# Kernel optimization log

Hardware: AMD Instinct MI355X
Metric: run time of the kernel (lower is better)

The kernel has to match this reference:

```python
import jax, jax.numpy as jnp
import numpy as np

C, INTER, RED4 = 256, 128, 64  # in_channels, inter_ch=max(C//2,32), C//4

def setup_inputs() -> dict:
    key = jax.random.key(0)
    ks = jax.random.split(key, 12)
    B, H, W = 8, 64, 64
    s = 0.02
    return {
        "x": jax.random.normal(ks[0], (B, C, H, W), dtype=jnp.float32),
        "theta_w": jax.random.normal(ks[1], (INTER, C), dtype=jnp.float32) * s,
        "phi_w": jax.random.normal(ks[2], (INTER, C), dtype=jnp.float32) * s,
        "g_w": jax.random.normal(ks[3], (INTER, C), dtype=jnp.float32) * s,
        "out_w": jax.random.normal(ks[4], (C, INTER), dtype=jnp.float32) * s,
        "bn_gamma": jnp.ones((C,), dtype=jnp.float32),
        "bn_beta": jnp.zeros((C,), dtype=jnp.float32),
        "fc1_w": jax.random.normal(ks[5], (RED4, C), dtype=jnp.float32) * s,
        "fc1_b": jnp.zeros((RED4,), dtype=jnp.float32),
        "fc2_w": jax.random.normal(ks[6], (C, RED4), dtype=jnp.float32) * s,
        "fc2_b": jnp.zeros((C,), dtype=jnp.float32),
    }

def reference(x, theta_w, phi_w, g_w, out_w, bn_gamma, bn_beta, fc1_w, fc1_b, fc2_w, fc2_b):
    B, Cc, H, W = x.shape
    N = H * W
    xf = x.reshape(B, Cc, N)                              # [B,C,N]
    # 1x1 convs == per-pixel matmuls
    theta = jnp.einsum('ic,bcn->bni', theta_w, xf)        # [B,N,I]
    phi = jnp.einsum('ic,bcn->bin', phi_w, xf)            # [B,I,N]
    g = jnp.einsum('ic,bcn->bni', g_w, xf)                # [B,N,I]
    scale = 1.0 / jnp.sqrt(jnp.asarray(theta.shape[-1], theta.dtype))
    attn = jax.nn.softmax(jnp.einsum('bni,bim->bnm', theta, phi) * scale, axis=-1)  # [B,N,N]
    out = jnp.einsum('bnm,bmi->bni', attn, g)             # [B,N,I]
    out = jnp.einsum('ci,bni->bcn', out_w, out).reshape(B, Cc, H, W)
    # BatchNorm2d (training mode: batch stats, biased variance, eps=1e-5)
    mean = out.mean(axis=(0, 2, 3))
    var = out.var(axis=(0, 2, 3))
    out = (out - mean[:, None, None]) * jax.lax.rsqrt(var[:, None, None] + 1e-5)
    out = out * bn_gamma[:, None, None] + bn_beta[:, None, None]
    # SE channel attention on the input x
    pooled = x.mean(axis=(2, 3))                          # [B,C]
    h = jax.nn.relu(pooled @ fc1_w.T + fc1_b)
    ch_w = jax.nn.sigmoid(h @ fc2_w.T + fc2_b)[:, :, None, None]
    return x + out * ch_w
```

## Files before the change

kernel.cpp:

```cpp
#include <hip/hip_runtime.h>

#define B_DIM 8
#define C_DIM 256
#define I_DIM 128
#define N_DIM 4096
#define R_DIM 64

typedef unsigned short u16;
typedef unsigned int u32;
typedef __attribute__((ext_vector_type(8))) __bf16 bf16x8;
typedef __attribute__((ext_vector_type(4))) float f32x4;
typedef __attribute__((ext_vector_type(16))) float f32x16;

union BF8 { u32 u[4]; bf16x8 v; };

__device__ __forceinline__ u16 f2bf(float f) {
    union { float f; u32 u; } v; v.f = f;
    u32 r = v.u + 0x7FFFu + ((v.u >> 16) & 1u);
    return (u16)(r >> 16);
}
__device__ __forceinline__ float bf2f(u16 h) {
    union { u32 u; float f; } v; v.u = (u32)h << 16; return v.f;
}
__device__ __forceinline__ u32 pk2(float a, float b) {
    return (u32)f2bf(a) | ((u32)f2bf(b) << 16);
}
__device__ __forceinline__ void async16(const u16* g, u16* l) {
    __builtin_amdgcn_global_load_lds((const __attribute__((address_space(1))) void*)g,
                                     (__attribute__((address_space(3))) void*)l, 16, 0, 0);
}

#define TH_SCALE 0.1275204890136f

static constexpr size_t OFF_BNSUM = 0;
static constexpr size_t OFF_BNSQ  = 1024;
static constexpr size_t OFF_POOL  = 2048;
static constexpr size_t OFF_CHW   = 10240;
static constexpr size_t OFF_W3    = 18432;
static constexpr size_t OFF_OWB   = 215040;
static constexpr size_t OFF_AO0   = 280576;
static constexpr size_t OFF_AO1   = OFF_AO0 + 8388608;
static constexpr size_t OFF_THETA = OFF_AO1 + 8388608;
static constexpr size_t OFF_PHIT  = OFF_THETA + 8388608;
static constexpr size_t OFF_GT    = OFF_PHIT + 8388608;
static constexpr size_t OFF_L0    = OFF_GT + 8388608;
static constexpr size_t OFF_L1    = OFF_L0 + 131072;
static constexpr size_t OFF_OUT2  = OFF_L1 + 131072;

__global__ void prep_kernel(const float* __restrict__ tw, const float* __restrict__ pw,
                            const float* __restrict__ gw, const float* __restrict__ ow,
                            u16* __restrict__ w3, u16* __restrict__ owb,
                            float* __restrict__ bnzero) {
    int idx = blockIdx.x * 256 + threadIdx.x;
    if (idx < 512) bnzero[idx] = 0.f;
    if (idx < 3 * 32768) {
        const float* src = idx < 32768 ? tw : (idx < 65536 ? pw : gw);
        w3[idx] = f2bf(src[idx & 32767]);
    }
    if (idx < 32768) owb[idx] = f2bf(ow[idx]);
}

__global__ void pool_kernel(const float* __restrict__ x, float* __restrict__ pooled) {
    int bc = blockIdx.x;
    const float4* row = (const float4*)(x + (size_t)bc * N_DIM);
    int t = threadIdx.x;
    float s = 0.f;
    for (int it = 0; it < 4; ++it) {
        float4 v = row[t + it * 256];
        s += v.x + v.y + v.z + v.w;
    }
    for (int d = 32; d; d >>= 1) s += __shfl_down(s, d);
    __shared__ float ls[4];
    if ((t & 63) == 0) ls[t >> 6] = s;
    __syncthreads();
    if (t == 0) pooled[bc] = (ls[0] + ls[1] + ls[2] + ls[3]) * (1.f / N_DIM);
}

__global__ void se_kernel(const float* __restrict__ pooled,
                          const float* __restrict__ fc1w, const float* __restrict__ fc1b,
                          const float* __restrict__ fc2w, const float* __restrict__ fc2b,
                          float* __restrict__ chw) {
    int b = blockIdx.x, t = threadIdx.x;
    __shared__ float sp[C_DIM], sh[R_DIM];
    sp[t] = pooled[b * C_DIM + t];
    __syncthreads();
    if (t < R_DIM) {
        float a = fc1b[t];
        for (int c = 0; c < C_DIM; ++c) a += sp[c] * fc1w[t * C_DIM + c];
        sh[t] = a > 0.f ? a : 0.f;
    }
    __syncthreads();
    float a = fc2b[t];
    for (int j = 0; j < R_DIM; ++j) a += sh[j] * fc2w[t * R_DIM + j];
    chw[b * C_DIM + t] = 1.f / (1.f + __builtin_amdgcn_exp2f(-a * 1.44269504089f));
}

__global__ __launch_bounds__(256) void qkv_kernel(const float* __restrict__ x,
                                                  const u16* __restrict__ w3,
                                                  u16* __restrict__ theta,
                                                  u16* __restrict__ phiT,
                                                  u16* __restrict__ gT) {
    const int bid = blockIdx.x;
    const int b = bid & 7, nt = bid >> 3;
    const int n0 = nt * 64;
    const int t = threadIdx.x, lane = t & 63, w = t >> 6;
    const int cl = lane & 31, h = lane >> 5;

    __shared__ u16 As[64 * 256];
    __shared__ u16 Ep[128 * 72];

    {
        const float* xb = x + ((size_t)b * C_DIM) * N_DIM + n0;
        for (int it = 0; it < 16; ++it) {
            int id = it * 256 + t;
            int c = id >> 4, l16 = id & 15;
            float4 v = *(const float4*)(xb + (size_t)c * N_DIM + l16 * 4);
            int g = c >> 3, co = c & 7;
            float vv[4] = {v.x, v.y, v.z, v.w};
            #pragma unroll
            for (int k = 0; k < 4; ++k) {
                int n = l16 * 4 + k;
                As[n * 256 + ((g ^ (n & 7)) << 3) + co] = f2bf(vv[k]);
            }
        }
    }
    __syncthreads();

    const int mt = w & 1;
    const int ip = w >> 1;
    bf16x8 afr[16];
    #pragma unroll
    for (int ks = 0; ks < 16; ++ks) {
        int r = mt * 32 + cl;
        int g = 2 * ks + h;
        afr[ks] = *(const bf16x8*)&As[r * 256 + ((g ^ (r & 7)) << 3)];
    }

    for (int z = 0; z < 3; ++z) {
        const u16* wz = w3 + z * (I_DIM * C_DIM);
        f32x16 acc[2] = {};
        #pragma unroll
        for (int ks = 0; ks < 16; ++ks) {
            #pragma unroll
            for (int f = 0; f < 2; ++f) {
                int irow = (2 * ip + f) * 32 + cl;
                bf16x8 bfr = *(const bf16x8*)(wz + (size_t)irow * C_DIM + ks * 16 + h * 8);
                acc[f] = __builtin_amdgcn_mfma_f32_32x32x16_bf16(afr[ks], bfr, acc[f], 0, 0, 0);
            }
        }
        if (z < 2) {
            float sc = (z == 0) ? TH_SCALE : 1.0f;
            #pragma unroll
            for (int f = 0; f < 2; ++f) {
                int i = (2 * ip + f) * 32 + cl;
                #pragma unroll
                for (int r2 = 0; r2 < 4; ++r2)
                    #pragma unroll
                    for (int e = 0; e < 4; ++e) {
                        int n = mt * 32 + 8 * r2 + 4 * h + e;
                        Ep[n * 136 + i] = f2bf(acc[f][4 * r2 + e] * sc);
                    }
            }
            __syncthreads();
            u16* dst = (z == 0) ? theta : phiT;
            #pragma unroll
            for (int it = 0; it < 4; ++it) {
                int id = it * 256 + t;
                int n = id >> 4, l16 = id & 15;
                f32x4 vv = *(const f32x4*)&Ep[n * 136 + l16 * 8];
                *(f32x4*)(dst + ((size_t)(b * N_DIM) + n0 + n) * I_DIM + l16 * 8) = vv;
            }
            __syncthreads();
        } else {
            #pragma unroll
            for (int f = 0; f < 2; ++f) {
                int i = (2 * ip + f) * 32 + cl;
                #pragma unroll
                for (int r2 = 0; r2 < 4; ++r2) {
                    u32 lo = pk2(acc[f][4 * r2 + 0], acc[f][4 * r2 + 1]);
                    u32 hi = pk2(acc[f][4 * r2 + 2], acc[f][4 * r2 + 3]);
                    int nb = mt * 32 + 8 * r2 + 4 * h;
                    *(u32*)&Ep[i * 72 + nb] = lo;
                    *(u32*)&Ep[i * 72 + nb + 2] = hi;
                }
            }
            __syncthreads();
            #pragma unroll
            for (int it = 0; it < 4; ++it) {
                int id = it * 256 + t;
                int i = id >> 3, l8 = id & 7;
                f32x4 vv = *(const f32x4*)&Ep[i * 72 + l8 * 8];
                *(f32x4*)(gT + ((size_t)(b * I_DIM) + i) * N_DIM + n0 + l8 * 8) = vv;
            }
        }
    }
}

__global__ __launch_bounds__(256) void attn_kernel(const u16* __restrict__ theta,
                                                   const u16* __restrict__ phiT,
                                                   const u16* __restrict__ gT,
                                                   u16* __restrict__ ao0, u16* __restrict__ ao1,
                                                   float* __restrict__ l0, float* __restrict__ l1) {
    const int bid = blockIdx.x;
    const int b = bid & 7, mh = (bid >> 3) & 1, qt = bid >> 4;
    const int t = threadIdx.x, lane = t & 63, w = t >> 6;
    const int cl = lane & 31, h = lane >> 5;
    const int qw = qt * 128 + w * 32;

    __shared__ u16 SM[16384];
    __shared__ float lex[4][32];
    u16* Ks = SM;
    u16* Vs = SM + 8192;

    bf16x8 qf[8];
    {
        const u16* qp = theta + ((size_t)(b * N_DIM) + qw + cl) * I_DIM + h * 8;
        #pragma unroll
        for (int ks = 0; ks < 8; ++ks) qf[ks] = *(const bf16x8*)(qp + ks * 16);
    }

    const u16* kbase = phiT + (size_t)b * N_DIM * I_DIM + (size_t)(mh * 2048) * I_DIM;
    const u16* vbase = gT + (size_t)b * I_DIM * N_DIM + mh * 2048;
    const u16* kptr[4]; const u16* vptr[4];
    #pragma unroll
    for (int it = 0; it < 4; ++it) {
        int gi = (w * 4 + it) * 64 + lane;
        int kr = gi >> 4, kg = gi & 15;
        kptr[it] = kbase + (size_t)kr * I_DIM + ((kg ^ (kr & 7)) << 3);
        int vr = gi >> 3, vg = gi & 7;
        vptr[it] = vbase + (size_t)vr * N_DIM + ((vg ^ (vr & 7)) << 3);
    }

    float lsum = 0.f;
    f32x16 O[4] = {};

    for (int mc = 0; mc < 32; ++mc) {
        __syncthreads();
        #pragma unroll
        for (int it = 0; it < 4; ++it) { async16(kptr[it], Ks + (w * 4 + it) * 512); kptr[it] += 64 * I_DIM; }
        #pragma unroll
        for (int it = 0; it < 4; ++it) { async16(vptr[it], Vs + (w * 4 + it) * 512); vptr[it] += 64; }
        __syncthreads();

        u32 pk[8][2];
        #pragma unroll
        for (int mt2 = 0; mt2 < 2; ++mt2) {
            f32x16 S = {};
            #pragma unroll
            for (int ks = 0; ks < 8; ++ks) {
                int r = mt2 * 32 + cl;
                bf16x8 kf = *(const bf16x8*)&Ks[r * 128 + (((2 * ks + h) ^ (r & 7)) << 3)];
                S = __builtin_amdgcn_mfma_f32_32x32x16_bf16(kf, qf[ks], S, 0, 0, 0);
            }
            #pragma unroll
            for (int r2 = 0; r2 < 4; ++r2) {
                float p0 = __builtin_amdgcn_exp2f(S[4 * r2 + 0]);
                float p1 = __builtin_amdgcn_exp2f(S[4 * r2 + 1]);
                float p2 = __builtin_amdgcn_exp2f(S[4 * r2 + 2]);
                float p3 = __builtin_amdgcn_exp2f(S[4 * r2 + 3]);
                lsum += (p0 + p1) + (p2 + p3);
                pk[mt2 * 4 + r2][0] = pk2(p0, p1);
                pk[mt2 * 4 + r2][1] = pk2(p2, p3);
            }
        }

        #pragma unroll
        for (int ks = 0; ks < 4; ++ks) {
            u32 a0 = pk[2 * ks][0], a1 = pk[2 * ks][1];
            u32 b0 = pk[2 * ks + 1][0], b1 = pk[2 * ks + 1][1];
            bool hb = (h != 0);
            u32 own0 = hb ? b0 : a0, own1 = hb ? b1 : a1;
            u32 xf0 = hb ? a0 : b0, xf1 = hb ? a1 : b1;
            u32 rc0 = (u32)__shfl_xor((int)xf0, 32);
            u32 rc1 = (u32)__shfl_xor((int)xf1, 32);
            BF8 A;
            A.u[0] = hb ? rc0 : own0;
            A.u[1] = hb ? rc1 : own1;
            A.u[2] = hb ? own0 : rc0;
            A.u[3] = hb ? own1 : rc1;
            #pragma unroll
            for (int f = 0; f < 4; ++f) {
                int ir = f * 32 + cl;
                bf16x8 vf = *(const bf16x8*)&Vs[ir * 64 + (((2 * ks + h) ^ (ir & 7)) << 3)];
                O[f] = __builtin_amdgcn_mfma_f32_32x32x16_bf16(A.v, vf, O[f], 0, 0, 0);
            }
        }
    }

    lsum += __shfl_xor(lsum, 32);
    if (h == 0) lex[w][cl] = lsum;
    __syncthreads();

    float linv[16];
    {
        float* lw = lex[w];
        #pragma unroll
        for (int r2 = 0; r2 < 4; ++r2) {
            f32x4 lv = *(const f32x4*)&lw[8 * r2 + 4 * h];
            #pragma unroll
            for (int e = 0; e < 4; ++e) linv[4 * r2 + e] = 1.f / lv[e];
        }
    }

    u16* aop = (mh == 0) ? ao0 : ao1;
    float* lp = (mh == 0) ? l0 : l1;
    if (h == 0) lp[(size_t)b * N_DIM + qw + cl] = lsum;

    u16* ep = SM + w * 4096;
    #pragma unroll
    for (int f = 0; f < 4; ++f)
        #pragma unroll
        for (int r2 = 0; r2 < 4; ++r2)
            #pragma unroll
            for (int e = 0; e < 4; ++e) {
                int q = 8 * r2 + 4 * h + e;
                ep[q * 128 + f * 32 + cl] = f2bf(O[f][4 * r2 + e] * linv[4 * r2 + e]);
            }
    __asm__ volatile("s_waitcnt lgkmcnt(0)" ::: "memory");
    #pragma unroll
    for (int it = 0; it < 8; ++it) {
        int id = it * 64 + lane;
        int q = id >> 4, l16 = id & 15;
        f32x4 vv = *(const f32x4*)&ep[q * 128 + l16 * 8];
        *(f32x4*)(aop + ((size_t)(b * N_DIM) + qw + q) * I_DIM + l16 * 8) = vv;
    }
}

__global__ __launch_bounds__(256) void oproj_kernel(const u16* __restrict__ ao0,
                                                    const u16* __restrict__ ao1,
                                                    const float* __restrict__ l0,
                                                    const float* __restrict__ l1,
                                                    const u16* __restrict__ owb,
                                                    u16* __restrict__ out2,
                                                    float* __restrict__ bnsum,
                                                    float* __restrict__ bnsumsq) {
    const int bid = blockIdx.x;
    const int b = bid & 7, nt = bid >> 3;
    const int n0 = nt * 64;
    const int t = threadIdx.x, lane = t & 63, w = t >> 6;
    const int cl = lane & 31, h = lane >> 5;

    __shared__ u16 Ep[256 * 72];
    __shared__ float lsum[C_DIM], lsq[C_DIM];
    lsum[t] = 0.f; lsq[t] = 0.f;
    __syncthreads();

    const int mt = w & 1;
    const int nn = n0 + mt * 32 + cl;
    float w0, w1;
    {
        float la = l0[(size_t)b * N_DIM + nn], lb = l1[(size_t)b * N_DIM + nn];
        float inv = 1.f / (la + lb);
        w0 = la * inv; w1 = lb * inv;
    }
    bf16x8 afr[8];
    {
        const u16* p0 = ao0 + ((size_t)(b * N_DIM) + nn) * I_DIM + h * 8;
        const u16* p1 = ao1 + ((size_t)(b * N_DIM) + nn) * I_DIM + h * 8;
        #pragma unroll
        for (int ks = 0; ks < 8; ++ks) {
            bf16x8 x0 = *(const bf16x8*)(p0 + ks * 16);
            bf16x8 x1 = *(const bf16x8*)(p1 + ks * 16);
            const u16* u0 = (const u16*)&x0;
            const u16* u1 = (const u16*)&x1;
            float c0 = w0 * bf2f(u0[0]) + w1 * bf2f(u1[0]);
            float c1 = w0 * bf2f(u0[1]) + w1 * bf2f(u1[1]);
            float c2 = w0 * bf2f(u0[2]) + w1 * bf2f(u1[2]);
            float c3 = w0 * bf2f(u0[3]) + w1 * bf2f(u1[3]);
            float c4 = w0 * bf2f(u0[4]) + w1 * bf2f(u1[4]);
            float c5 = w0 * bf2f(u0[5]) + w1 * bf2f(u1[5]);
            float c6 = w0 * bf2f(u0[6]) + w1 * bf2f(u1[6]);
            float c7 = w0 * bf2f(u0[7]) + w1 * bf2f(u1[7]);
            BF8 r;
            r.u[0] = pk2(c0, c1); r.u[1] = pk2(c2, c3);
            r.u[2] = pk2(c4, c5); r.u[3] = pk2(c6, c7);
            afr[ks] = r.v;
        }
    }

    f32x16 D[4] = {};
    #pragma unroll
    for (int ks = 0; ks < 8; ++ks) {
        #pragma unroll
        for (int j = 0; j < 4; ++j) {
            int cr = ((w >> 1) * 4 + j) * 32 + cl;
            bf16x8 bfr = *(const bf16x8*)(owb + (size_t)cr * I_DIM + ks * 16 + h * 8);
            D[j] = __builtin_amdgcn_mfma_f32_32x32x16_bf16(afr[ks], bfr, D[j], 0, 0, 0);
        }
    }

    #pragma unroll
    for (int j = 0; j < 4; ++j) {
        int c = ((w >> 1) * 4 + j) * 32 + cl;
        float s1 = 0.f, s2 = 0.f;
        #pragma unroll
        for (int r2 = 0; r2 < 4; ++r2) {
            float v0 = D[j][4 * r2 + 0], v1 = D[j][4 * r2 + 1];
            float v2 = D[j][4 * r2 + 2], v3 = D[j][4 * r2 + 3];
            s1 += (v0 + v1) + (v2 + v3);
            s2 += (v0 * v0 + v1 * v1) + (v2 * v2 + v3 * v3);
            int nb = mt * 32 + 8 * r2 + 4 * h;
            *(u32*)&Ep[c * 72 + nb] = pk2(v0, v1);
            *(u32*)&Ep[c * 72 + nb + 2] = pk2(v2, v3);
        }
        atomicAdd(&lsum[c], s1);
        atomicAdd(&lsq[c], s2);
    }
    __syncthreads();
    #pragma unroll
    for (int it = 0; it < 8; ++it) {
        int id = it * 256 + t;
        int c = id >> 3, l8 = id & 7;
        f32x4 vv = *(const f32x4*)&Ep[c * 72 + l8 * 8];
        *(f32x4*)(out2 + ((size_t)(b * C_DIM) + c) * N_DIM + n0 + l8 * 8) = vv;
    }
    atomicAdd(&bnsum[t], lsum[t]);
    atomicAdd(&bnsumsq[t], lsq[t]);
}

__global__ void final_kernel(const float* __restrict__ x, const u16* __restrict__ out2,
                             const float* __restrict__ bnsum, const float* __restrict__ bnsumsq,
                             const float* __restrict__ gamma, const float* __restrict__ beta,
                             const float* __restrict__ chw, float* __restrict__ out) {
    int idx = blockIdx.x * 256 + threadIdx.x;
    int e = idx * 4;
    int b = e >> 20;
    int c = (e >> 12) & 255;
    float mean = bnsum[c] * (1.f / 32768.f);
    float var = bnsumsq[c] * (1.f / 32768.f) - mean * mean;
    float sc = gamma[c] * rsqrtf(var + 1e-5f);
    float sh = beta[c] - mean * sc;
    float cw = chw[b * C_DIM + c];
    ushort4 o16 = ((const ushort4*)out2)[idx];
    float4 xv = ((const float4*)x)[idx];
    float4 res;
    res.x = xv.x + (bf2f(o16.x) * sc + sh) * cw;
    res.y = xv.y + (bf2f(o16.y) * sc + sh) * cw;
    res.z = xv.z + (bf2f(o16.z) * sc + sh) * cw;
    res.w = xv.w + (bf2f(o16.w) * sc + sh) * cw;
    ((float4*)out)[idx] = res;
}

extern "C" void kernel_launch(void* const* d_in, const int* in_sizes, int n_in,
                              void* d_out, int out_size, void* d_ws, size_t ws_size,
                              hipStream_t stream) {
    const float* x   = (const float*)d_in[0];
    const float* tw  = (const float*)d_in[1];
    const float* pw  = (const float*)d_in[2];
    const float* gw  = (const float*)d_in[3];
    const float* ow  = (const float*)d_in[4];
    const float* gam = (const float*)d_in[5];
    const float* bet = (const float*)d_in[6];
    const float* f1w = (const float*)d_in[7];
    const float* f1b = (const float*)d_in[8];
    const float* f2w = (const float*)d_in[9];
    const float* f2b = (const float*)d_in[10];
    float* out = (float*)d_out;

    char* ws = (char*)d_ws;
    float* bnsum   = (float*)(ws + OFF_BNSUM);
    float* bnsumsq = (float*)(ws + OFF_BNSQ);
    float* pooled  = (float*)(ws + OFF_POOL);
    float* chw     = (float*)(ws + OFF_CHW);
    u16*   w3      = (u16*)(ws + OFF_W3);
    u16*   owb     = (u16*)(ws + OFF_OWB);
    u16*   ao0     = (u16*)(ws + OFF_AO0);
    u16*   ao1     = (u16*)(ws + OFF_AO1);
    u16*   theta   = (u16*)(ws + OFF_THETA);
    u16*   phiT    = (u16*)(ws + OFF_PHIT);
    u16*   gT      = (u16*)(ws + OFF_GT);
    float* l0      = (float*)(ws + OFF_L0);
    float* l1      = (float*)(ws + OFF_L1);
    u16*   out2    = (u16*)(ws + OFF_OUT2);

    prep_kernel<<<384, 256, 0, stream>>>(tw, pw, gw, ow, w3, owb, bnsum);
    pool_kernel<<<B_DIM * C_DIM, 256, 0, stream>>>(x, pooled);
    se_kernel<<<B_DIM, 256, 0, stream>>>(pooled, f1w, f1b, f2w, f2b, chw);
    qkv_kernel<<<512, 256, 0, stream>>>(x, w3, theta, phiT, gT);
    attn_kernel<<<512, 256, 0, stream>>>(theta, phiT, gT, ao0, ao1, l0, l1);
    oproj_kernel<<<512, 256, 0, stream>>>(ao0, ao1, l0, l1, owb, out2, bnsum, bnsumsq);
    final_kernel<<<8192, 256, 0, stream>>>(x, out2, bnsum, bnsumsq, gam, bet, chw, out);
}
```

Baseline: 294.6 us.

## Double-buffer attention K/V loads, fuse pooling into QKV, truncate bf16 packing

The attention kernel now double-buffers K/V tiles in LDS. It prefetches the next chunk with async global-to-LDS loads while the current one is computed, using raw s_barrier and vmcnt waits instead of two __syncthreads per iteration. The SE average pooling is folded into the QKV kernel via shuffle reductions and atomicAdd, which removes a separate pass over x. Softmax probabilities are packed to bf16 by truncation with a perm instruction instead of round-to-nearest, trading a little precision for fewer ALU ops. A final __syncthreads is replaced by an lgkmcnt wait, which may be unsafe across waves reading lex.

```diff
diff --git a/kernel.cpp b/kernel.cpp
--- a/kernel.cpp
+++ b/kernel.cpp
@@ -24,6 +24,10 @@
 }
 __device__ __forceinline__ u32 pk2(float a, float b) {
     return (u32)f2bf(a) | ((u32)f2bf(b) << 16);
+}
+__device__ __forceinline__ u32 pk2t(float a, float b) {
+    union { float f; u32 u; } ua, ub; ua.f = a; ub.f = b;
+    return __builtin_amdgcn_perm(ub.u, ua.u, 0x07060302u);
 }
 __device__ __forceinline__ void async16(const u16* g, u16* l) {
     __builtin_amdgcn_global_load_lds((const __attribute__((address_space(1))) void*)g,
@@ -50,30 +54,15 @@
 __global__ void prep_kernel(const float* __restrict__ tw, const float* __restrict__ pw,
                             const float* __restrict__ gw, const float* __restrict__ ow,
                             u16* __restrict__ w3, u16* __restrict__ owb,
-                            float* __restrict__ bnzero) {
+                            float* __restrict__ bnzero, float* __restrict__ pooled) {
     int idx = blockIdx.x * 256 + threadIdx.x;
     if (idx < 512) bnzero[idx] = 0.f;
+    if (idx < 2048) pooled[idx] = 0.f;
     if (idx < 3 * 32768) {
         const float* src = idx < 32768 ? tw : (idx < 65536 ? pw : gw);
         w3[idx] = f2bf(src[idx & 32767]);
     }
     if (idx < 32768) owb[idx] = f2bf(ow[idx]);
-}
-
-__global__ void pool_kernel(const float* __restrict__ x, float* __restrict__ pooled) {
-    int bc = blockIdx.x;
-    const float4* row = (const float4*)(x + (size_t)bc * N_DIM);
-    int t = threadIdx.x;
-    float s = 0.f;
-    for (int it = 0; it < 4; ++it) {
-        float4 v = row[t + it * 256];
-        s += v.x + v.y + v.z + v.w;
-    }
-    for (int d = 32; d; d >>= 1) s += __shfl_down(s, d);
-    __shared__ float ls[4];
-    if ((t & 63) == 0) ls[t >> 6] = s;
-    __syncthreads();
-    if (t == 0) pooled[bc] = (ls[0] + ls[1] + ls[2] + ls[3]) * (1.f / N_DIM);
 }
 
 __global__ void se_kernel(const float* __restrict__ pooled,
@@ -82,7 +71,7 @@
                           float* __restrict__ chw) {
     int b = blockIdx.x, t = threadIdx.x;
     __shared__ float sp[C_DIM], sh[R_DIM];
-    sp[t] = pooled[b * C_DIM + t];
+    sp[t] = pooled[b * C_DIM + t] * (1.f / N_DIM);
     __syncthreads();
     if (t < R_DIM) {
         float a = fc1b[t];
@@ -99,7 +88,8 @@
                                                   const u16* __restrict__ w3,
                                                   u16* __restrict__ theta,
                                                   u16* __restrict__ phiT,
-                                                  u16* __restrict__ gT) {
+                                                  u16* __restrict__ gT,
+                                                  float* __restrict__ pooled) {
     const int bid = blockIdx.x;
     const int b = bid & 7, nt = bid >> 3;
     const int n0 = nt * 64;
@@ -122,6 +112,10 @@
                 int n = l16 * 4 + k;
                 As[n * 256 + ((g ^ (n & 7)) << 3) + co] = f2bf(vv[k]);
             }
+            float s = (v.x + v.y) + (v.z + v.w);
+            s += __shfl_xor(s, 1); s += __shfl_xor(s, 2);
+            s += __shfl_xor(s, 4); s += __shfl_xor(s, 8);
+            if ((t & 15) == 0) atomicAdd(&pooled[b * C_DIM + c], s);
         }
     }
     __syncthreads();
@@ -207,10 +201,8 @@
     const int cl = lane & 31, h = lane >> 5;
     const int qw = qt * 128 + w * 32;
 
-    __shared__ u16 SM[16384];
+    __shared__ u16 SM[32768];
     __shared__ float lex[4][32];
-    u16* Ks = SM;
-    u16* Vs = SM + 8192;
 
     bf16x8 qf[8];
     {
@@ -231,16 +223,33 @@
         vptr[it] = vbase + (size_t)vr * N_DIM + ((vg ^ (vr & 7)) << 3);
     }
 
+    auto issue = [&](int p) {
+        u16* Kd = SM + p * 16384;
+        u16* Vd = SM + p * 16384 + 8192;
+        #pragma unroll
+        for (int it = 0; it < 4; ++it) { async16(kptr[it], Kd + (w * 4 + it) * 512); kptr[it] += 64 * I_DIM; }
+        #pragma unroll
+        for (int it = 0; it < 4; ++it) { async16(vptr[it], Vd + (w * 4 + it) * 512); vptr[it] += 64; }
+    };
+
     float lsum = 0.f;
     f32x16 O[4] = {};
 
+    issue(0);
+
     for (int mc = 0; mc < 32; ++mc) {
-        __syncthreads();
-        #pragma unroll
-        for (int it = 0; it < 4; ++it) { async16(kptr[it], Ks + (w * 4 + it) * 512); kptr[it] += 64 * I_DIM; }
-        #pragma unroll
-        for (int it = 0; it < 4; ++it) { async16(vptr[it], Vs + (w * 4 + it) * 512); vptr[it] += 64; }
-        __syncthreads();
+        const int p = mc & 1;
+        __asm__ volatile("s_barrier" ::: "memory");
+        if (mc < 31) {
+            issue(1 - p);
+            __asm__ volatile("s_waitcnt vmcnt(8)" ::: "memory");
+        } else {
+            __asm__ volatile("s_waitcnt vmcnt(0)" ::: "memory");
+        }
+        __asm__ volatile("s_barrier" ::: "memory");
+
+        const u16* Ks = SM + p * 16384;
+        const u16* Vs = SM + p * 16384 + 8192;
 
         u32 pk[8][2];
         #pragma unroll
@@ -259,8 +268,8 @@
                 float p2 = __builtin_amdgcn_exp2f(S[4 * r2 + 2]);
                 float p3 = __builtin_amdgcn_exp2f(S[4 * r2 + 3]);
                 lsum += (p0 + p1) + (p2 + p3);
-                pk[mt2 * 4 + r2][0] = pk2(p0, p1);
-                pk[mt2 * 4 + r2][1] = pk2(p2, p3);
+                pk[mt2 * 4 + r2][0] = pk2t(p0, p1);
+                pk[mt2 * 4 + r2][1] = pk2t(p2, p3);
             }
         }
 
@@ -289,7 +298,7 @@
 
     lsum += __shfl_xor(lsum, 32);
     if (h == 0) lex[w][cl] = lsum;
-    __syncthreads();
+    __asm__ volatile("s_waitcnt lgkmcnt(0)" ::: "memory");
 
     float linv[16];
     {
@@ -473,10 +482,9 @@
     float* l1      = (float*)(ws + OFF_L1);
     u16*   out2    = (u16*)(ws + OFF_OUT2);
 
-    prep_kernel<<<384, 256, 0, stream>>>(tw, pw, gw, ow, w3, owb, bnsum);
-    pool_kernel<<<B_DIM * C_DIM, 256, 0, stream>>>(x, pooled);
+    prep_kernel<<<384, 256, 0, stream>>>(tw, pw, gw, ow, w3, owb, bnsum, pooled);
+    qkv_kernel<<<512, 256, 0, stream>>>(x, w3, theta, phiT, gT, pooled);
     se_kernel<<<B_DIM, 256, 0, stream>>>(pooled, f1w, f1b, f2w, f2b, chw);
-    qkv_kernel<<<512, 256, 0, stream>>>(x, w3, theta, phiT, gT);
     attn_kernel<<<512, 256, 0, stream>>>(theta, phiT, gT, ao0, ao1, l0, l1);
     oproj_kernel<<<512, 256, 0, stream>>>(ao0, ao1, l0, l1, owb, out2, bnsum, bnsumsq);
     final_kernel<<<8192, 256, 0, stream>>>(x, out2, bnsum, bnsumsq, gam, bet, chw, out);
```

Result: faster. 270.4 us (-8.2%).
